# Kernel optimization log

Measured on AMD Instinct MI355X. Metric: run time of the kernel, lower is better.

Reference implementation:

```python
import jax, jax.numpy as jnp
import numpy as np

N, E, EDGES, G = 4096, 256, 131072, 64
H, DH = 4, 64  # MHA heads, head dim


def _ln(x, g, b, eps=1e-5):
    m = jnp.mean(x, -1, keepdims=True)
    v = jnp.var(x, -1, keepdims=True)
    return g * (x - m) * jax.lax.rsqrt(v + eps) + b


def setup_inputs() -> dict:
    key = jax.random.key(0)
    ks = jax.random.split(key, 40)
    i = iter(range(40))
    def rn(shape, s=1.0):
        return jax.random.normal(ks[next(i)], shape, jnp.float32) * s
    w = lambda shape: rn(shape, 0.02)
    inp = {
        "node_hidden": rn((N, E)),
        "edge_hidden": rn((EDGES, E)),
        "pos": rn((N, 3)),
        # GINEConv MLP: Lin(E,2E) -> LN -> ReLU -> Dropout -> Lin(2E,E)
        "gine_w1": w((E, 2 * E)), "gine_b1": jnp.zeros((2 * E,)),
        "gine_ln_g": jnp.ones((2 * E,)), "gine_ln_b": jnp.zeros((2 * E,)),
        "gine_w2": w((2 * E, E)), "gine_b2": jnp.zeros((E,)),
        "norm1_g": jnp.ones((E,)), "norm1_b": jnp.zeros((E,)),
        # DirectionalMessagePassing params
        "dir_w": w((3, E)), "dir_b": jnp.zeros((E,)),
        "msg_w": w((E, E)), "msg_b": jnp.zeros((E,)),
        # MultiheadAttention
        "wq": w((E, E)), "bq": jnp.zeros((E,)),
        "wk": w((E, E)), "bk": jnp.zeros((E,)),
        "wv": w((E, E)), "bv": jnp.zeros((E,)),
        "wo": w((E, E)), "bo": jnp.zeros((E,)),
        # gate
        "gate_w": w((2 * E, E)), "gate_b": jnp.zeros((E,)),
        "norm2_g": jnp.ones((E,)), "norm2_b": jnp.zeros((E,)),
        # GraphNorm affine
        "gn_g": jnp.ones((E,)), "gn_b": jnp.zeros((E,)),
        # int inputs
        "edge_index": jax.random.randint(ks[next(i)], (2, EDGES), 0, N, jnp.int64 if jax.config.jax_enable_x64 else jnp.int32),
        "node_id": jnp.sort(jax.random.randint(ks[next(i)], (N,), 0, G)),
        "edge_id": jax.random.randint(ks[next(i)], (EDGES,), 0, G),
    }
    return inp


def reference(node_hidden, edge_hidden, pos,
              gine_w1, gine_b1, gine_ln_g, gine_ln_b, gine_w2, gine_b2,
              norm1_g, norm1_b, dir_w, dir_b, msg_w, msg_b,
              wq, bq, wk, bk, wv, bv, wo, bo,
              gate_w, gate_b, norm2_g, norm2_b, gn_g, gn_b,
              edge_index, node_id, edge_id):
    src, dst = edge_index[0], edge_index[1]
    identity = node_hidden

    # --- GINEConv: out = MLP(x + sum_j relu(x_j + e_ij)), eps=0 ---
    msg = jax.nn.relu(node_hidden[src] + edge_hidden)           # [EDGES, E]
    agg = jax.ops.segment_sum(msg, dst, num_segments=N)         # [N, E]
    h = node_hidden + agg
    h = jax.nn.relu(_ln(h @ gine_w1 + gine_b1, gine_ln_g, gine_ln_b))
    gnn_out = _ln(h @ gine_w2 + gine_b2, norm1_g, norm1_b)      # norm1

    # --- DirectionalMessagePassing over unit edge directions ---
    vec = pos[dst] - pos[src]                                   # [EDGES, 3]
    vec = vec / (jnp.linalg.norm(vec, axis=-1, keepdims=True) + 1e-8)
    dfeat = vec @ dir_w + dir_b                                 # [EDGES, E]
    smsg = gnn_out[src] * dfeat
    sagg = jax.ops.segment_sum(smsg, dst, num_segments=N)
    spatial_out = sagg @ msg_w + msg_b                          # [N, E]

    # --- MHA: q = gnn_out, k = v = spatial_out (seq = nodes, batch=1) ---
    q = (gnn_out @ wq + bq).reshape(N, H, DH)
    k = (spatial_out @ wk + bk).reshape(N, H, DH)
    v = (spatial_out @ wv + bv).reshape(N, H, DH)
    scores = jnp.einsum("nhd,mhd->hnm", q, k) / np.sqrt(DH)
    attn = jax.nn.softmax(scores, axis=-1)
    fused = jnp.einsum("hnm,mhd->nhd", attn, v).reshape(N, E) @ wo + bo

    # --- gated residual blend + norm2 ---
    gate = jax.nn.sigmoid(jnp.concatenate([fused, identity], -1) @ gate_w + gate_b)
    out = gate * fused + (1.0 - gate) * identity
    out = _ln(out, norm2_g, norm2_b)

    # --- GraphNorm: per-graph mean/var over nodes (segment stats) ---
    counts = jax.ops.segment_sum(jnp.ones((N, 1), out.dtype), node_id, num_segments=G)
    mean = jax.ops.segment_sum(out, node_id, num_segments=G) / counts
    cen = out - mean[node_id]
    var = jax.ops.segment_sum(cen * cen, node_id, num_segments=G) / counts
    out = gn_g * cen * jax.lax.rsqrt(var[node_id] + 1e-5) + gn_b

    # last_act = True; dropout is eval-mode identity
    return jax.nn.relu(out)
```

## Files before the change

kernel.cpp:

```cpp
#include <hip/hip_runtime.h>
#include <hip/hip_bf16.h>

#define N_NODES 4096
#define E_DIM   256
#define N_EDGES 131072
#define N_GRAPHS 64
#define H_HEADS 4
#define DH      64
#define SPLIT   8

typedef unsigned short u16;
typedef __attribute__((ext_vector_type(8))) short bf16x8;
typedef __attribute__((ext_vector_type(4))) float f32x4;

__device__ __forceinline__ float u2f(u16 u) {
    union { unsigned int i; float f; } c; c.i = ((unsigned int)u) << 16; return c.f;
}
__device__ __forceinline__ u16 f2bu(float f) {
    __hip_bfloat16 h = __float2bfloat16(f);
    return *reinterpret_cast<u16*>(&h);
}
__device__ __forceinline__ float ldv(const void* p, size_t i, int f32) {
    return f32 ? ((const float*)p)[i] : u2f(((const u16*)p)[i]);
}
__device__ __forceinline__ float4 ldv4(const void* p, size_t i, int f32) {
    if (f32) return *(const float4*)((const float*)p + i);
    ushort4 u = *(const ushort4*)((const u16*)p + i);
    return make_float4(u2f(u.x), u2f(u.y), u2f(u.z), u2f(u.w));
}
__device__ __forceinline__ int ldi(const int* p, int i, int i64) {
    return i64 ? p[2 * i] : p[i];
}

__global__ void k_detect(const u16* __restrict__ ones_raw, const int* __restrict__ ei_raw,
                         int* __restrict__ flags) {
    flags[0] = (ones_raw[0] == 0) ? 1 : 0;
    flags[1] = (ei_raw[1] == 0 && ei_raw[3] == 0 && ei_raw[5] == 0 && ei_raw[7] == 0) ? 1 : 0;
}

__global__ void k_cvt(const void* __restrict__ s, float* __restrict__ d, int n,
                      const int* __restrict__ flags) {
    int i = blockIdx.x * 256 + threadIdx.x;
    if (i < n) d[i] = ldv(s, i, flags[0]);
}

__global__ void k_cvtb(const void* __restrict__ s, u16* __restrict__ d, int n4,
                       const int* __restrict__ flags) {
    int i = blockIdx.x * 256 + threadIdx.x;
    if (i < n4) {
        float4 v = ldv4(s, (size_t)i * 4, flags[0]);
        ushort4 o;
        o.x = f2bu(v.x); o.y = f2bu(v.y); o.z = f2bu(v.z); o.w = f2bu(v.w);
        ((ushort4*)d)[i] = o;
    }
}

struct SmDesc { const void* src; float* dst; int n; };
struct SmTable { SmDesc d[19]; };
__global__ __launch_bounds__(256) void k_cvts(SmTable tb, const int* __restrict__ flags) {
    int ti = blockIdx.x / 48;
    int off = (blockIdx.x % 48) * 256 + threadIdx.x;
    SmDesc e = tb.d[ti];
    if (off < e.n) e.dst[off] = ldv(e.src, off, flags[0]);
}

struct WtDesc { const void* src; u16* dst; int K; int N; int base; };
struct WtTable { WtDesc d[8]; };
__global__ __launch_bounds__(256) void k_cvtw(WtTable tb, const int* __restrict__ flags) {
    __shared__ u16 tile[64][68];
    int b = blockIdx.x;
    int i = 0;
    while (i < 7 && b >= tb.d[i + 1].base) i++;
    WtDesc e = tb.d[i];
    int tl = b - e.base;
    int ntn = e.N >> 6;
    int kt = tl / ntn, nt = tl % ntn;
    int t = threadIdx.x, r = t >> 2, c0 = (t & 3) * 16;
    int f32 = flags[0];
#pragma unroll
    for (int j = 0; j < 16; j++)
        tile[r][c0 + j] = f2bu(ldv(e.src, (size_t)(kt * 64 + r) * e.N + nt * 64 + c0 + j, f32));
    __syncthreads();
#pragma unroll
    for (int j = 0; j < 16; j++)
        e.dst[(size_t)(nt * 64 + r) * e.K + kt * 64 + c0 + j] = tile[c0 + j][r];
}

__global__ __launch_bounds__(256) void k_biasfold(const float* __restrict__ bq, const float* __restrict__ bk,
                                                  const float* __restrict__ bv, const float* __restrict__ msgb,
                                                  const u16* __restrict__ wkvt, float* __restrict__ bqkv) {
    int t = blockIdx.x * 256 + threadIdx.x;
    if (t < 256) { bqkv[t] = bq[t]; return; }
    int c = t - 256;
    float s = (c < 256) ? bk[c] : bv[c - 256];
    const u16* row = wkvt + (size_t)c * 256;
    float acc = 0.f;
    for (int k = 0; k < 256; k++) acc = fmaf(msgb[k], u2f(row[k]), acc);
    bqkv[256 + c] = s + acc;
}

__global__ __launch_bounds__(256) void k_mgemm(const void* __restrict__ A0, const void* __restrict__ A1,
                                               int K0, int Ktot, const u16* __restrict__ BT,
                                               const float* __restrict__ bias, void* __restrict__ C,
                                               int Nc, int outbf, int abf, int mode,
                                               u16* __restrict__ vt) {
    __shared__ u16 As[64 * 64];
    __shared__ u16 Bs[64 * 64];
    int t = threadIdx.x;
    int wv = t >> 6, l = t & 63, lg = l >> 4, lc = l & 15;
    int wm = wv >> 1, wn = wv & 1;
    int m0 = blockIdx.y * 64, n0 = blockIdx.x * 64;
    f32x4 acc[2][2] = {};
    int sr = t >> 2, sc = (t & 3) * 16;
    int sw = (sr & 7) << 3;

    for (int k0 = 0; k0 < Ktot; k0 += 64) {
        const void* Abase; int astride, kof;
        if (mode == 1) { Abase = (n0 < K0) ? A0 : A1; astride = Ktot; kof = k0; }
        else if (k0 < K0) { Abase = A0; astride = K0; kof = k0; }
        else { Abase = A1; astride = Ktot - K0; kof = k0 - K0; }
        if (abf) {
            const u16* Ap = (const u16*)Abase + (size_t)(m0 + sr) * astride + kof + sc;
            *(bf16x8*)&As[(sr * 64 + sc) ^ sw]     = *(const bf16x8*)Ap;
            *(bf16x8*)&As[(sr * 64 + sc + 8) ^ sw] = *(const bf16x8*)(Ap + 8);
        } else {
            const float* Ap = (const float*)Abase + (size_t)(m0 + sr) * astride + kof + sc;
#pragma unroll
            for (int j = 0; j < 2; j++) {
                float4 f0 = *(const float4*)(Ap + j * 8);
                float4 f1 = *(const float4*)(Ap + j * 8 + 4);
                bf16x8 bv;
                bv[0] = (short)f2bu(f0.x); bv[1] = (short)f2bu(f0.y);
                bv[2] = (short)f2bu(f0.z); bv[3] = (short)f2bu(f0.w);
                bv[4] = (short)f2bu(f1.x); bv[5] = (short)f2bu(f1.y);
                bv[6] = (short)f2bu(f1.z); bv[7] = (short)f2bu(f1.w);
                *(bf16x8*)&As[(sr * 64 + sc + j * 8) ^ sw] = bv;
            }
        }
        const u16* Bp = BT + (size_t)(n0 + sr) * Ktot + k0 + sc;
        *(bf16x8*)&Bs[(sr * 64 + sc) ^ sw]     = *(const bf16x8*)Bp;
        *(bf16x8*)&Bs[(sr * 64 + sc + 8) ^ sw] = *(const bf16x8*)(Bp + 8);
        __syncthreads();
#pragma unroll
        for (int ks = 0; ks < 2; ks++) {
            bf16x8 af[2], bfr[2];
#pragma unroll
            for (int mi = 0; mi < 2; mi++) {
                int row = wm * 32 + mi * 16 + lc;
                af[mi] = *(const bf16x8*)&As[(row * 64 + ks * 32 + lg * 8) ^ ((row & 7) << 3)];
            }
#pragma unroll
            for (int ni = 0; ni < 2; ni++) {
                int col = wn * 32 + ni * 16 + lc;
                bfr[ni] = *(const bf16x8*)&Bs[(col * 64 + ks * 32 + lg * 8) ^ ((col & 7) << 3)];
            }
#pragma unroll
            for (int mi = 0; mi < 2; mi++)
#pragma unroll
                for (int ni = 0; ni < 2; ni++)
                    acc[mi][ni] = __builtin_amdgcn_mfma_f32_16x16x32_bf16(af[mi], bfr[ni], acc[mi][ni], 0, 0, 0);
        }
        __syncthreads();
    }
#pragma unroll
    for (int mi = 0; mi < 2; mi++)
#pragma unroll
        for (int ni = 0; ni < 2; ni++) {
            int col = n0 + wn * 32 + ni * 16 + lc;
            float bb = bias ? bias[col] : 0.f;
#pragma unroll
            for (int r = 0; r < 4; r++) {
                int row = m0 + wm * 32 + mi * 16 + lg * 4 + r;
                float v = acc[mi][ni][r] + bb;
                u16 hb = f2bu(v);
                if (outbf) ((u16*)C)[(size_t)row * Nc + col] = hb;
                else       ((float*)C)[(size_t)row * Nc + col] = v;
                if (vt && col >= 512) vt[(size_t)(col - 512) * N_NODES + row] = hb;
            }
        }
// ... 89 lines not shown
            for (int n = 0; n < 4; n++)
                P_lds[wv][(q * 64 + n * 16 + lc) ^ sw] = f2bu(p[n][r]);
        }
#pragma unroll
        for (int kc = 0; kc < 2; kc++) {
            bf16x8 a = *(const bf16x8*)&P_lds[wv][(lc * 64 + kc * 32 + lg * 8) ^ ((lc & 7) << 3)];
#pragma unroll
            for (int n = 0; n < 4; n++) {
                int row = n * 16 + lc;
                bf16x8 b = *(const bf16x8*)&V_lds[(row * 64 + kc * 32 + lg * 8) ^ ((row & 7) << 3)];
                oacc[n] = __builtin_amdgcn_mfma_f32_16x16x32_bf16(a, b, oacc[n], 0, 0, 0);
            }
        }
    }

#pragma unroll
    for (int r = 0; r < 4; r++) {
        u16* pp = part + ((size_t)(c * H_HEADS + h) * N_NODES + q0 + lg * 4 + r) * 72;
#pragma unroll
        for (int n = 0; n < 4; n++) pp[n * 16 + lc] = f2bu(oacc[n][r]);
        if (lc == 0) { *(float*)(pp + 64) = mrow[r]; *(float*)(pp + 66) = lrow[r]; }
    }
}

__global__ __launch_bounds__(256) void k_combine(const u16* __restrict__ part, u16* __restrict__ attnoh) {
    int n = blockIdx.x, t = threadIdx.x;
    int h = t >> 6, d = t & 63;
    float M = -1e30f;
#pragma unroll
    for (int c = 0; c < SPLIT; c++)
        M = fmaxf(M, *(const float*)(part + ((size_t)(c * H_HEADS + h) * N_NODES + n) * 72 + 64));
    float L = 0.f, o = 0.f;
#pragma unroll
    for (int c = 0; c < SPLIT; c++) {
        const u16* pp = part + ((size_t)(c * H_HEADS + h) * N_NODES + n) * 72;
        float w = __expf(*(const float*)(pp + 64) - M);
        L = fmaf(*(const float*)(pp + 66), w, L);
        o = fmaf(u2f(pp[d]), w, o);
    }
    attnoh[(size_t)n * E_DIM + h * DH + d] = f2bu(o / L);
}

__device__ __forceinline__ void block_red2(float& a, float& b, float* sbuf) {
#pragma unroll
    for (int o = 32; o > 0; o >>= 1) { a += __shfl_down(a, o); b += __shfl_down(b, o); }
    int w = threadIdx.x >> 6;
    if ((threadIdx.x & 63) == 0) { sbuf[w] = a; sbuf[4 + w] = b; }
    __syncthreads();
    a = sbuf[0] + sbuf[1] + sbuf[2] + sbuf[3];
    b = sbuf[4] + sbuf[5] + sbuf[6] + sbuf[7];
    __syncthreads();
}

__global__ void k_count(const int* __restrict__ ei, int* __restrict__ count,
                        const int* __restrict__ flags) {
    int e = blockIdx.x * 256 + threadIdx.x;
    int i64 = flags[1];
    int d = i64 ? ei[2 * (N_EDGES + e)] : ei[N_EDGES + e];
    atomicAdd(&count[d], 1);
}

__global__ __launch_bounds__(1024) void k_scan(const int* __restrict__ count,
                                               int* __restrict__ offs, int* __restrict__ cursor) {
    __shared__ int wsum[16];
    int t = threadIdx.x, lane = t & 63, wid = t >> 6;
    int c0 = count[t * 4 + 0], c1 = count[t * 4 + 1], c2 = count[t * 4 + 2], c3 = count[t * 4 + 3];
    int tot = c0 + c1 + c2 + c3;
    int inc = tot;
#pragma unroll
    for (int o = 1; o < 64; o <<= 1) { int v = __shfl_up(inc, o); if (lane >= o) inc += v; }
    if (lane == 63) wsum[wid] = inc;
    __syncthreads();
    if (t < 16) {
        int v = wsum[t];
#pragma unroll
        for (int o = 1; o < 16; o <<= 1) { int u = __shfl_up(v, o); if (t >= o) v += u; }
        wsum[t] = v;
    }
    __syncthreads();
    int base = (wid ? wsum[wid - 1] : 0) + inc - tot;
    int o0 = base, o1 = base + c0, o2 = o1 + c1, o3 = o2 + c2;
    offs[t * 4 + 0] = o0; offs[t * 4 + 1] = o1; offs[t * 4 + 2] = o2; offs[t * 4 + 3] = o3;
    cursor[t * 4 + 0] = o0; cursor[t * 4 + 1] = o1; cursor[t * 4 + 2] = o2; cursor[t * 4 + 3] = o3;
    if (t == 1023) offs[4096] = wsum[15];
}

__global__ void k_scatter(const int* __restrict__ ei, int* __restrict__ cursor,
                          int* __restrict__ elist, const int* __restrict__ flags) {
    int e = blockIdx.x * 256 + threadIdx.x;
    int i64 = flags[1];
    int d = i64 ? ei[2 * (N_EDGES + e)] : ei[N_EDGES + e];
    int p = atomicAdd(&cursor[d], 1);
    elist[p] = e;
}

__global__ __launch_bounds__(256) void k_gine_agg(const float* __restrict__ xf, const void* __restrict__ eh,
                                                  const int* __restrict__ ei, const int* __restrict__ offs,
                                                  const int* __restrict__ elist, const int* __restrict__ flags,
                                                  float* __restrict__ hout) {
    int wv = threadIdx.x >> 6, ld = threadIdx.x & 63;
    int n = blockIdx.x * 4 + wv;
    int f32 = flags[0], i64 = flags[1];
    int cc = ld * 4;
    float4 acc = *(const float4*)&xf[(size_t)n * E_DIM + cc];
    int i0 = offs[n], i1 = offs[n + 1];
    int i = i0;
    for (; i + 4 <= i1; i += 4) {
        int e[4], s[4];
#pragma unroll
        for (int j = 0; j < 4; j++) e[j] = elist[i + j];
#pragma unroll
        for (int j = 0; j < 4; j++) s[j] = ldi(ei, e[j], i64);
        float4 a[4], x[4];
#pragma unroll
        for (int j = 0; j < 4; j++) a[j] = ldv4(eh, (size_t)e[j] * E_DIM + cc, f32);
#pragma unroll
        for (int j = 0; j < 4; j++) x[j] = *(const float4*)&xf[(size_t)s[j] * E_DIM + cc];
#pragma unroll
        for (int j = 0; j < 4; j++) {
            acc.x += fmaxf(x[j].x + a[j].x, 0.f);
            acc.y += fmaxf(x[j].y + a[j].y, 0.f);
            acc.z += fmaxf(x[j].z + a[j].z, 0.f);
            acc.w += fmaxf(x[j].w + a[j].w, 0.f);
        }
    }
    for (; i < i1; i++) {
        int e0 = elist[i];
        int s0 = ldi(ei, e0, i64);
        float4 a0 = ldv4(eh, (size_t)e0 * E_DIM + cc, f32);
        float4 x0 = *(const float4*)&xf[(size_t)s0 * E_DIM + cc];
        acc.x += fmaxf(x0.x + a0.x, 0.f);
        acc.y += fmaxf(x0.y + a0.y, 0.f);
        acc.z += fmaxf(x0.z + a0.z, 0.f);
        acc.w += fmaxf(x0.w + a0.w, 0.f);
    }
    *(float4*)&hout[(size_t)n * E_DIM + cc] = acc;
}

template <int W>
__global__ __launch_bounds__(256) void k_ln(float* __restrict__ X, const float* __restrict__ g,
                                            const float* __restrict__ b, int relu) {
    __shared__ float sbuf[8];
    constexpr int PE = W / 256;
    int n = blockIdx.x, t = threadIdx.x;
    float* row = X + (size_t)n * W;
    float x[PE];
    float s = 0.f, s2 = 0.f;
#pragma unroll
    for (int i = 0; i < PE; i++) { x[i] = row[t + i * 256]; s += x[i]; s2 += x[i] * x[i]; }
    block_red2(s, s2, sbuf);
    float mean = s / W;
    float var = fmaxf(s2 / W - mean * mean, 0.f);
    float rstd = rsqrtf(var + 1e-5f);
#pragma unroll
    for (int i = 0; i < PE; i++) {
        int c = t + i * 256;
        float y = g[c] * (x[i] - mean) * rstd + b[c];
        if (relu) y = fmaxf(y, 0.f);
        row[c] = y;
    }
}

__global__ __launch_bounds__(256) void k_dir(const float* __restrict__ posf, const int* __restrict__ ei,
                                             const int* __restrict__ offs, const int* __restrict__ elist,
                                             const int* __restrict__ flags,
                                             const float* __restrict__ gnn, const float* __restrict__ dw,
                                             const float* __restrict__ db, float* __restrict__ sagg) {
    int wv = threadIdx.x >> 6, ld = threadIdx.x & 63;
    int n = blockIdx.x * 4 + wv;
    int i64 = flags[1];
    int cc = ld * 4;
    float4 w0 = *(const float4*)&dw[cc];
    float4 w1 = *(const float4*)&dw[256 + cc];
    float4 w2 = *(const float4*)&dw[512 + cc];
    float4 bb = *(const float4*)&db[cc];
    float px = posf[n * 3 + 0], py = posf[n * 3 + 1], pz = posf[n * 3 + 2];
    float4 acc = {0.f, 0.f, 0.f, 0.f};
    int i0 = offs[n], i1 = offs[n + 1];
    int i = i0;
    for (; i + 2 <= i1; i += 2) {
        int e0 = elist[i], e1 = elist[i + 1];
        int s0 = ldi(ei, e0, i64), s1 = ldi(ei, e1, i64);
        float q0x = posf[s0 * 3 + 0], q0y = posf[s0 * 3 + 1], q0z = posf[s0 * 3 + 2];
        float q1x = posf[s1 * 3 + 0], q1y = posf[s1 * 3 + 1], q1z = posf[s1 * 3 + 2];
        float4 g0 = *(const float4*)&gnn[(size_t)s0 * E_DIM + cc];
        float4 g1 = *(const float4*)&gnn[(size_t)s1 * E_DIM + cc];
        float vx0 = px - q0x, vy0 = py - q0y, vz0 = pz - q0z;
        float vx1 = px - q1x, vy1 = py - q1y, vz1 = pz - q1z;
        float rn0 = 1.f / (sqrtf(vx0 * vx0 + vy0 * vy0 + vz0 * vz0) + 1e-8f);
        float rn1 = 1.f / (sqrtf(vx1 * vx1 + vy1 * vy1 + vz1 * vz1) + 1e-8f);
        acc.x = fmaf(g0.x, bb.x + (vx0 * w0.x + vy0 * w1.x + vz0 * w2.x) * rn0, acc.x);
        acc.y = fmaf(g0.y, bb.y + (vx0 * w0.y + vy0 * w1.y + vz0 * w2.y) * rn0, acc.y);
        acc.z = fmaf(g0.z, bb.z + (vx0 * w0.z + vy0 * w1.z + vz0 * w2.z) * rn0, acc.z);
        acc.w = fmaf(g0.w, bb.w + (vx0 * w0.w + vy0 * w1.w + vz0 * w2.w) * rn0, acc.w);
        acc.x = fmaf(g1.x, bb.x + (vx1 * w0.x + vy1 * w1.x + vz1 * w2.x) * rn1, acc.x);
        acc.y = fmaf(g1.y, bb.y + (vx1 * w0.y + vy1 * w1.y + vz1 * w2.y) * rn1, acc.y);
        acc.z = fmaf(g1.z, bb.z + (vx1 * w0.z + vy1 * w1.z + vz1 * w2.z) * rn1, acc.z);
        acc.w = fmaf(g1.w, bb.w + (vx1 * w0.w + vy1 * w1.w + vz1 * w2.w) * rn1, acc.w);
    }
    if (i < i1) {
        int e0 = elist[i];
        int s0 = ldi(ei, e0, i64);
        float q0x = posf[s0 * 3 + 0], q0y = posf[s0 * 3 + 1], q0z = posf[s0 * 3 + 2];
        float4 g0 = *(const float4*)&gnn[(size_t)s0 * E_DIM + cc];
        float vx0 = px - q0x, vy0 = py - q0y, vz0 = pz - q0z;
        float rn0 = 1.f / (sqrtf(vx0 * vx0 + vy0 * vy0 + vz0 * vz0) + 1e-8f);
        acc.x = fmaf(g0.x, bb.x + (vx0 * w0.x + vy0 * w1.x + vz0 * w2.x) * rn0, acc.x);
        acc.y = fmaf(g0.y, bb.y + (vx0 * w0.y + vy0 * w1.y + vz0 * w2.y) * rn0, acc.y);
        acc.z = fmaf(g0.z, bb.z + (vx0 * w0.z + vy0 * w1.z + vz0 * w2.z) * rn0, acc.z);
        acc.w = fmaf(g0.w, bb.w + (vx0 * w0.w + vy0 * w1.w + vz0 * w2.w) * rn0, acc.w);
    }
    *(float4*)&sagg[(size_t)n * E_DIM + cc] = acc;
}

__global__ __launch_bounds__(256) void k_gate_ln(const float* __restrict__ gl, const float* __restrict__ fused,
                                                 const float* __restrict__ xf, const float* __restrict__ g2,
                                                 const float* __restrict__ b2, float* __restrict__ out2) {
    __shared__ float sbuf[8];
    int n = blockIdx.x, t = threadIdx.x;
    float z = gl[(size_t)n * E_DIM + t];
    float gate = 1.f / (1.f + __expf(-z));
    float o = gate * fused[(size_t)n * E_DIM + t] + (1.f - gate) * xf[(size_t)n * E_DIM + t];
    float s = o, s2 = o * o;
    block_red2(s, s2, sbuf);
    float mean = s / E_DIM;
    float var = fmaxf(s2 / E_DIM - mean * mean, 0.f);
    float y = g2[t] * (o - mean) * rsqrtf(var + 1e-5f) + b2[t];
    out2[(size_t)n * E_DIM + t] = y;
}

__device__ __forceinline__ int lbound(const int* __restrict__ nid, int v, int i64) {
    int lo = 0, hi = N_NODES;
    while (lo < hi) { int mid = (lo + hi) >> 1; if (ldi(nid, mid, i64) < v) lo = mid + 1; else hi = mid; }
    return lo;
}

__global__ __launch_bounds__(256) void k_gnstats(const int* __restrict__ nid, const int* __restrict__ flags,
                                                 const float* __restrict__ out2,
                                                 float* __restrict__ gnm, float* __restrict__ gnr) {
    int g = blockIdx.x, t = threadIdx.x;
    int i64 = flags[1];
    int a = lbound(nid, g, i64), bnd = lbound(nid, g + 1, i64);
    int cnt = bnd - a;
    float s = 0.f, s2 = 0.f;
    for (int n = a; n < bnd; n++) {
        float x = out2[(size_t)n * E_DIM + t];
        s += x; s2 = fmaf(x, x, s2);
    }
    float inv = cnt ? 1.f / (float)cnt : 0.f;
    float mean = s * inv;
    float var = fmaxf(s2 * inv - mean * mean, 0.f);
    gnm[g * E_DIM + t] = mean;
    gnr[g * E_DIM + t] = rsqrtf(var + 1e-5f);
}

__global__ __launch_bounds__(256) void k_gnapply(const float* __restrict__ out2, const int* __restrict__ nid,
                                                 const float* __restrict__ gnm, const float* __restrict__ gnr,
                                                 const float* __restrict__ gg, const float* __restrict__ gb,
                                                 const int* __restrict__ flags, void* __restrict__ out) {
    int n = blockIdx.x, t = threadIdx.x;
    int g = ldi(nid, n, flags[1]);
    float y = gg[t] * (out2[(size_t)n * E_DIM + t] - gnm[g * E_DIM + t]) * gnr[g * E_DIM + t] + gb[t];
    y = fmaxf(y, 0.f);
    size_t idx = (size_t)n * E_DIM + t;
    if (flags[0]) ((float*)out)[idx] = y;
    else ((__hip_bfloat16*)out)[idx] = __float2bfloat16(y);
}

extern "C" void kernel_launch(void* const* d_in, const int* in_sizes, int n_in,
                              void* d_out, int out_size, void* d_ws, size_t ws_size,
                              hipStream_t stream) {
    const void* x_r    = d_in[0];
    const void* eh_r   = d_in[1];
    const void* pos_r  = d_in[2];
    const void* w1_r   = d_in[3];
    const void* b1_r   = d_in[4];
    const void* glng_r = d_in[5];
    const void* glnb_r = d_in[6];
    const void* w2_r   = d_in[7];
    const void* b2_r   = d_in[8];
    const void* n1g_r  = d_in[9];
    const void* n1b_r  = d_in[10];
    const void* dirw_r = d_in[11];
    const void* dirb_r = d_in[12];
    const void* msgw_r = d_in[13];
    const void* msgb_r = d_in[14];
    const void* wq_r   = d_in[15];
    const void* bq_r   = d_in[16];
    const void* wk_r   = d_in[17];
    const void* bk_r   = d_in[18];
    const void* wv_r   = d_in[19];
    const void* bv_r   = d_in[20];
    const void* wo_r   = d_in[21];
    const void* bo_r   = d_in[22];
    const void* gw_r   = d_in[23];
    const void* gb_r   = d_in[24];
    const void* n2g_r  = d_in[25];
    const void* n2b_r  = d_in[26];
    const void* gng_r  = d_in[27];
    const void* gnb_r  = d_in[28];
    const int* ei      = (const int*)d_in[29];
    const int* nid     = (const int*)d_in[30];

    char* ws = (char*)d_ws;
    const size_t KB = 1 << 10, MB = 1 << 20;
    int*   flags  = (int*)(ws + 0);
    int*   count  = (int*)(ws + 16 * KB);
    int*   offs   = (int*)(ws + 32 * KB);
    int*   cursor = (int*)(ws + 64 * KB);
    int*   elist  = (int*)(ws + 128 * KB);

    float* posf   = (float*)(ws + 1 * MB);
    float* prm    = (float*)(ws + 1 * MB + 64 * KB);
    float* b1f   = prm + 0;
    float* glngf = prm + 512,  *glnbf = prm + 1024;
    float* b2f   = prm + 1536;
    float* n1gf  = prm + 1792, *n1bf  = prm + 2048;
    float* dirwf = prm + 2304;
    float* dirbf = prm + 3072, *msgbf = prm + 3328;
    float* bqf   = prm + 3584, *bkf   = prm + 3840, *bvf = prm + 4096, *bof = prm + 4352;
    float* gbf   = prm + 4608;
    float* n2gf  = prm + 4864, *n2bf  = prm + 5120;
    float* gngf  = prm + 5376, *gnbf  = prm + 5632;

    u16* w1t    = (u16*)(ws + 2 * MB);
    u16* w2t    = (u16*)(ws + 2 * MB + 256 * KB);
    u16* wot    = (u16*)(ws + 2 * MB + 512 * KB);
    u16* gwt    = (u16*)(ws + 2 * MB + 640 * KB);
    u16* wqkvt  = (u16*)(ws + 3 * MB);
    u16* wkvt   = (u16*)(ws + 3 * MB + 384 * KB);
    u16* msgwb  = (u16*)(ws + 3 * MB + 640 * KB);
    float* bqkvf = (float*)(ws + 3 * MB + 768 * KB);

    float* xf     = (float*)(ws + 5 * MB);
    float* hbuf   = (float*)(ws + 9 * MB);
    float* T1     = (float*)(ws + 13 * MB);
    float* gnn    = (float*)(ws + 21 * MB);
    float* sagg   = (float*)(ws + 25 * MB);
    u16*   QKVh   = (u16*)(ws + 29 * MB);
    u16*   VT     = (u16*)(ws + 35 * MB);
    u16*   part   = (u16*)(ws + 37 * MB);
    u16*   attnoh = (u16*)(ws + 9 * MB);
    float* fused  = (float*)(ws + 13 * MB);
    float* gatel  = (float*)(ws + 17 * MB);
    float* out2   = (float*)(ws + 21 * MB);
    float* gnm    = (float*)(ws + 25 * MB);
    float* gnr    = (float*)(ws + 25 * MB + 64 * KB);

    k_detect<<<1, 1, 0, stream>>>((const u16*)glng_r, ei, flags);

    k_cvt<<<(N_NODES * E_DIM + 255) / 256, 256, 0, stream>>>(x_r, xf, N_NODES * E_DIM, flags);

    SmTable st;
    {
        int i = 0;
        auto add = [&](const void* s, float* d, int n) { st.d[i].src = s; st.d[i].dst = d; st.d[i].n = n; i++; };
        add(pos_r, posf, N_NODES * 3);
        add(b1_r, b1f, 512); add(glng_r, glngf, 512); add(glnb_r, glnbf, 512);
        add(b2_r, b2f, 256); add(n1g_r, n1gf, 256); add(n1b_r, n1bf, 256);
        add(dirw_r, dirwf, 768); add(dirb_r, dirbf, 256); add(msgb_r, msgbf, 256);
        add(bq_r, bqf, 256); add(bk_r, bkf, 256); add(bv_r, bvf, 256); add(bo_r, bof, 256);
        add(gb_r, gbf, 256); add(n2g_r, n2gf, 256); add(n2b_r, n2bf, 256);
        add(gng_r, gngf, 256); add(gnb_r, gnbf, 256);
    }
    k_cvts<<<19 * 48, 256, 0, stream>>>(st, flags);

    WtTable wt;
    {
        int i = 0, base = 0;
        auto add = [&](const void* s, u16* d, int K, int N) {
            wt.d[i].src = s; wt.d[i].dst = d; wt.d[i].K = K; wt.d[i].N = N; wt.d[i].base = base;
            base += (K / 64) * (N / 64); i++;
        };
        add(w1_r, w1t, 256, 512);
        add(w2_r, w2t, 512, 256);
        add(wq_r, wqkvt, 256, 256);
        add(wk_r, wkvt, 256, 256);
        add(wv_r, wkvt + 256 * 256, 256, 256);
        add(wo_r, wot, 256, 256);
        add(gw_r, gwt, 512, 256);
        wt.d[7].base = 0x7fffffff;
        k_cvtw<<<base, 256, 0, stream>>>(wt, flags);
    }
    k_cvtb<<<64, 256, 0, stream>>>(msgw_r, msgwb, 256 * 256 / 4, flags);
    k_mgemm<<<dim3(4, 8), 256, 0, stream>>>(wkvt, nullptr, 256, 256, msgwb, nullptr,
                                            wqkvt + 256 * 256, 256, 1, 1, 0, nullptr);
    k_biasfold<<<3, 256, 0, stream>>>(bqf, bkf, bvf, msgbf, wkvt, bqkvf);

    hipMemsetAsync(count, 0, N_NODES * sizeof(int), stream);
    k_count<<<N_EDGES / 256, 256, 0, stream>>>(ei, count, flags);
    k_scan<<<1, 1024, 0, stream>>>(count, offs, cursor);
    k_scatter<<<N_EDGES / 256, 256, 0, stream>>>(ei, cursor, elist, flags);

    k_gine_agg<<<N_NODES / 4, 256, 0, stream>>>(xf, eh_r, ei, offs, elist, flags, hbuf);
    k_mgemm<<<dim3(8, 64), 256, 0, stream>>>(hbuf, nullptr, 256, 256, w1t, b1f, T1, 512, 0, 0, 0, nullptr);
    k_ln<512><<<N_NODES, 256, 0, stream>>>(T1, glngf, glnbf, 1);
    k_mgemm<<<dim3(4, 64), 256, 0, stream>>>(T1, nullptr, 512, 512, w2t, b2f, gnn, 256, 0, 0, 0, nullptr);
    k_ln<256><<<N_NODES, 256, 0, stream>>>(gnn, n1gf, n1bf, 0);

    k_dir<<<N_NODES / 4, 256, 0, stream>>>(posf, ei, offs, elist, flags, gnn, dirwf, dirbf, sagg);

    k_mgemm<<<dim3(12, 64), 256, 0, stream>>>(gnn, sagg, 256, 256, wqkvt, bqkvf, QKVh, 768, 1, 0, 1, VT);

    k_attn<<<dim3(N_NODES / 64, H_HEADS, SPLIT), 256, 0, stream>>>(QKVh, VT, part);
    k_combine<<<N_NODES, 256, 0, stream>>>(part, attnoh);
    k_mgemm<<<dim3(4, 64), 256, 0, stream>>>(attnoh, nullptr, 256, 256, wot, bof, fused, 256, 0, 1, 0, nullptr);

    k_mgemm<<<dim3(4, 64), 256, 0, stream>>>(fused, xf, 256, 512, gwt, gbf, gatel, 256, 0, 0, 0, nullptr);
    k_gate_ln<<<N_NODES, 256, 0, stream>>>(gatel, fused, xf, n2gf, n2bf, out2);

    k_gnstats<<<N_GRAPHS, 256, 0, stream>>>(nid, flags, out2, gnm, gnr);
    k_gnapply<<<N_NODES, 256, 0, stream>>>(out2, nid, gnm, gnr, gngf, gnbf, flags, d_out);
}
```

Baseline: 292.2 us.

## Merge prep kernels, fold wo into gate GEMM, use bf16 gathers, halve attention split

Replaces the separate detect/convert kernels with one k_prep launch and makes each kernel recompute the dtype flags inline. The output projection wo is folded algebraically into the gate weights, so a single GEMM produces both fused and gate logits. Gathers now read bf16 copies of x and gnn, plus packed (edge, src) pairs and padded pos4, which cuts gather bandwidth and one level of indirection. The attention split drops from 8 to 4. The trade-off is slightly lower precision and extra weight-folding GEMMs in setup.

```diff
diff --git a/kernel.cpp b/kernel.cpp
--- a/kernel.cpp
+++ b/kernel.cpp
@@ -7,7 +7,7 @@
 #define N_GRAPHS 64
 #define H_HEADS 4
 #define DH      64
-#define SPLIT   8
+#define SPLIT   4
 
 typedef unsigned short u16;
 typedef __attribute__((ext_vector_type(8))) short bf16x8;
@@ -28,82 +28,117 @@
     ushort4 u = *(const ushort4*)((const u16*)p + i);
     return make_float4(u2f(u.x), u2f(u.y), u2f(u.z), u2f(u.w));
 }
+__device__ __forceinline__ float4 ldb4(const u16* p, size_t i) {
+    ushort4 u = *(const ushort4*)(p + i);
+    return make_float4(u2f(u.x), u2f(u.y), u2f(u.z), u2f(u.w));
+}
+__device__ __forceinline__ int chk_f32(const void* ones_raw) { return ((const u16*)ones_raw)[0] == 0; }
+__device__ __forceinline__ int chk_i64(const int* ei) {
+    return (ei[1] == 0 && ei[3] == 0 && ei[5] == 0 && ei[7] == 0);
+}
 __device__ __forceinline__ int ldi(const int* p, int i, int i64) {
     return i64 ? p[2 * i] : p[i];
 }
 
-__global__ void k_detect(const u16* __restrict__ ones_raw, const int* __restrict__ ei_raw,
-                         int* __restrict__ flags) {
-    flags[0] = (ones_raw[0] == 0) ? 1 : 0;
-    flags[1] = (ei_raw[1] == 0 && ei_raw[3] == 0 && ei_raw[5] == 0 && ei_raw[7] == 0) ? 1 : 0;
-}
-
-__global__ void k_cvt(const void* __restrict__ s, float* __restrict__ d, int n,
-                      const int* __restrict__ flags) {
-    int i = blockIdx.x * 256 + threadIdx.x;
-    if (i < n) d[i] = ldv(s, i, flags[0]);
-}
-
-__global__ void k_cvtb(const void* __restrict__ s, u16* __restrict__ d, int n4,
-                       const int* __restrict__ flags) {
-    int i = blockIdx.x * 256 + threadIdx.x;
-    if (i < n4) {
-        float4 v = ldv4(s, (size_t)i * 4, flags[0]);
-        ushort4 o;
-        o.x = f2bu(v.x); o.y = f2bu(v.y); o.z = f2bu(v.z); o.w = f2bu(v.w);
-        ((ushort4*)d)[i] = o;
-    }
-}
-
 struct SmDesc { const void* src; float* dst; int n; };
-struct SmTable { SmDesc d[19]; };
-__global__ __launch_bounds__(256) void k_cvts(SmTable tb, const int* __restrict__ flags) {
-    int ti = blockIdx.x / 48;
-    int off = (blockIdx.x % 48) * 256 + threadIdx.x;
-    SmDesc e = tb.d[ti];
-    if (off < e.n) e.dst[off] = ldv(e.src, off, flags[0]);
-}
-
+struct SmTable { SmDesc d[18]; };
 struct WtDesc { const void* src; u16* dst; int K; int N; int base; };
 struct WtTable { WtDesc d[8]; };
-__global__ __launch_bounds__(256) void k_cvtw(WtTable tb, const int* __restrict__ flags) {
+
+__global__ __launch_bounds__(256) void k_prep(const void* __restrict__ x_r, float* __restrict__ xf,
+                                              u16* __restrict__ xh, const void* __restrict__ pos_r,
+                                              float4* __restrict__ pos4, SmTable st, WtTable wt,
+                                              const void* __restrict__ msgw_r, u16* __restrict__ msgwb,
+                                              const void* __restrict__ wo_r, u16* __restrict__ wob,
+                                              const void* __restrict__ ones_raw) {
     __shared__ u16 tile[64][68];
-    int b = blockIdx.x;
-    int i = 0;
-    while (i < 7 && b >= tb.d[i + 1].base) i++;
-    WtDesc e = tb.d[i];
-    int tl = b - e.base;
-    int ntn = e.N >> 6;
-    int kt = tl / ntn, nt = tl % ntn;
-    int t = threadIdx.x, r = t >> 2, c0 = (t & 3) * 16;
-    int f32 = flags[0];
-#pragma unroll
-    for (int j = 0; j < 16; j++)
-        tile[r][c0 + j] = f2bu(ldv(e.src, (size_t)(kt * 64 + r) * e.N + nt * 64 + c0 + j, f32));
-    __syncthreads();
-#pragma unroll
-    for (int j = 0; j < 16; j++)
-        e.dst[(size_t)(nt * 64 + r) * e.K + kt * 64 + c0 + j] = tile[c0 + j][r];
-}
-
-__global__ __launch_bounds__(256) void k_biasfold(const float* __restrict__ bq, const float* __restrict__ bk,
-                                                  const float* __restrict__ bv, const float* __restrict__ msgb,
-                                                  const u16* __restrict__ wkvt, float* __restrict__ bqkv) {
-    int t = blockIdx.x * 256 + threadIdx.x;
-    if (t < 256) { bqkv[t] = bq[t]; return; }
-    int c = t - 256;
-    float s = (c < 256) ? bk[c] : bv[c - 256];
-    const u16* row = wkvt + (size_t)c * 256;
-    float acc = 0.f;
-    for (int k = 0; k < 256; k++) acc = fmaf(msgb[k], u2f(row[k]), acc);
-    bqkv[256 + c] = s + acc;
+    int b = blockIdx.x, t = threadIdx.x;
+    int f32 = chk_f32(ones_raw);
+    if (b < 4096) {
+        int i = b * 256 + t;
+        float v = ldv(x_r, i, f32);
+        xf[i] = v; xh[i] = f2bu(v);
+        return;
+    }
+    b -= 4096;
+    if (b < 16) {
+        int n = b * 256 + t;
+        pos4[n] = make_float4(ldv(pos_r, n * 3 + 0, f32), ldv(pos_r, n * 3 + 1, f32),
+                              ldv(pos_r, n * 3 + 2, f32), 0.f);
+        return;
+    }
+    b -= 16;
+    if (b < 18 * 48) {
+        int ti = b / 48;
+        int off = (b % 48) * 256 + t;
+        SmDesc e = st.d[ti];
+        if (off < e.n) e.dst[off] = ldv(e.src, off, f32);
+        return;
+    }
+    b -= 18 * 48;
+    if (b < 160) {
+        int i = 0;
+        while (i < 7 && b >= wt.d[i + 1].base) i++;
+        WtDesc e = wt.d[i];
+        int tl = b - e.base;
+        int ntn = e.N >> 6;
+        int kt = tl / ntn, nt = tl % ntn;
+        int r = t >> 2, c0 = (t & 3) * 16;
+#pragma unroll
+        for (int j = 0; j < 16; j++)
+            tile[r][c0 + j] = f2bu(ldv(e.src, (size_t)(kt * 64 + r) * e.N + nt * 64 + c0 + j, f32));
+        __syncthreads();
+#pragma unroll
+        for (int j = 0; j < 16; j++)
+            e.dst[(size_t)(nt * 64 + r) * e.K + kt * 64 + c0 + j] = tile[c0 + j][r];
+        return;
+    }
+    b -= 160;
+    if (b < 256) { int i = b * 256 + t; msgwb[i] = f2bu(ldv(msgw_r, i, f32)); return; }
+    b -= 256;
+    { int i = b * 256 + t; wob[i] = f2bu(ldv(wo_r, i, f32)); }
+}
+
+__global__ __launch_bounds__(256) void k_asm2(const u16* __restrict__ wot, const u16* __restrict__ foldT,
+                                              const u16* __restrict__ gwt, u16* __restrict__ BT2) {
+    int idx = blockIdx.x * 256 + threadIdx.x;
+    int col = idx >> 9, k = idx & 511;
+    u16 v;
+    if (col < 256) v = (k < 256) ? wot[col * 256 + k] : (u16)0;
+    else { int c = col - 256; v = (k < 256) ? foldT[c * 256 + k] : gwt[(size_t)c * 512 + k]; }
+    BT2[idx] = v;
+}
+
+__global__ __launch_bounds__(256) void k_biases(const float* __restrict__ bqf, const float* __restrict__ bkf,
+                                                const float* __restrict__ bvf, const float* __restrict__ msgbf,
+                                                const u16* __restrict__ wkvt, const float* __restrict__ bof,
+                                                const float* __restrict__ gbf, const u16* __restrict__ gwt,
+                                                float* __restrict__ bqkv, float* __restrict__ bias2) {
+    int b = blockIdx.x, t = threadIdx.x;
+    if (b < 3) {
+        int i = b * 256 + t;
+        if (i < 256) { bqkv[i] = bqf[i]; return; }
+        int c = i - 256;
+        float s = (c < 256) ? bkf[c] : bvf[c - 256];
+        const u16* row = wkvt + (size_t)c * 256;
+        float acc = 0.f;
+        for (int k = 0; k < 256; k++) acc = fmaf(msgbf[k], u2f(row[k]), acc);
+        bqkv[256 + c] = s + acc;
+    } else if (b == 3) {
+        bias2[t] = bof[t];
+    } else {
+        float acc = gbf[t];
+        const u16* row = gwt + (size_t)t * 512;
+        for (int j = 0; j < 256; j++) acc = fmaf(bof[j], u2f(row[j]), acc);
+        bias2[256 + t] = acc;
+    }
 }
 
 __global__ __launch_bounds__(256) void k_mgemm(const void* __restrict__ A0, const void* __restrict__ A1,
+                                               int as0, int as1, int abf0, int abf1,
                                                int K0, int Ktot, const u16* __restrict__ BT,
                                                const float* __restrict__ bias, void* __restrict__ C,
-                                               int Nc, int outbf, int abf, int mode,
-                                               u16* __restrict__ vt) {
+                                               int Nc, int outbf, int mode, u16* __restrict__ vt) {
     __shared__ u16 As[64 * 64];
     __shared__ u16 Bs[64 * 64];
     int t = threadIdx.x;
@@ -115,16 +150,16 @@
     int sw = (sr & 7) << 3;
 
     for (int k0 = 0; k0 < Ktot; k0 += 64) {
-        const void* Abase; int astride, kof;
-        if (mode == 1) { Abase = (n0 < K0) ? A0 : A1; astride = Ktot; kof = k0; }
-        else if (k0 < K0) { Abase = A0; astride = K0; kof = k0; }
-        else { Abase = A1; astride = Ktot - K0; kof = k0 - K0; }
+        const void* Ab; int astr, kof, abf;
+        if (mode == 1) { int pick = (n0 < K0); Ab = pick ? A0 : A1; astr = pick ? as0 : as1; abf = pick ? abf0 : abf1; kof = k0; }
+        else if (k0 < K0) { Ab = A0; astr = as0; abf = abf0; kof = k0; }
+        else { Ab = A1; astr = as1; abf = abf1; kof = k0 - K0; }
         if (abf) {
-            const u16* Ap = (const u16*)Abase + (size_t)(m0 + sr) * astride + kof + sc;
+            const u16* Ap = (const u16*)Ab + (size_t)(m0 + sr) * astr + kof + sc;
             *(bf16x8*)&As[(sr * 64 + sc) ^ sw]     = *(const bf16x8*)Ap;
             *(bf16x8*)&As[(sr * 64 + sc + 8) ^ sw] = *(const bf16x8*)(Ap + 8);
         } else {
-            const float* Ap = (const float*)Abase + (size_t)(m0 + sr) * astride + kof + sc;
+            const float* Ap = (const float*)Ab + (size_t)(m0 + sr) * astr + kof + sc;
 #pragma unroll
             for (int j = 0; j < 2; j++) {
                 float4 f0 = *(const float4*)(Ap + j * 8);
@@ -320,10 +355,9 @@
     __syncthreads();
 }
 
-__global__ void k_count(const int* __restrict__ ei, int* __restrict__ count,
-                        const int* __restrict__ flags) {
+__global__ void k_count(const int* __restrict__ ei, int* __restrict__ count) {
     int e = blockIdx.x * 256 + threadIdx.x;
-    int i64 = flags[1];
+    int i64 = chk_i64(ei);
     int d = i64 ? ei[2 * (N_EDGES + e)] : ei[N_EDGES + e];
     atomicAdd(&count[d], 1);
 }
@@ -354,36 +388,35 @@
 }
 
 __global__ void k_scatter(const int* __restrict__ ei, int* __restrict__ cursor,
-                          int* __restrict__ elist, const int* __restrict__ flags) {
+                          int2* __restrict__ elist2) {
     int e = blockIdx.x * 256 + threadIdx.x;
-    int i64 = flags[1];
+    int i64 = chk_i64(ei);
+    int s = i64 ? ei[2 * e] : ei[e];
     int d = i64 ? ei[2 * (N_EDGES + e)] : ei[N_EDGES + e];
     int p = atomicAdd(&cursor[d], 1);
-    elist[p] = e;
-}
-
-__global__ __launch_bounds__(256) void k_gine_agg(const float* __restrict__ xf, const void* __restrict__ eh,
-                                                  const int* __restrict__ ei, const int* __restrict__ offs,
-                                                  const int* __restrict__ elist, const int* __restrict__ flags,
-                                                  float* __restrict__ hout) {
+    elist2[p] = make_int2(e, s);
+}
+
+__global__ __launch_bounds__(256) void k_gine_agg(const float* __restrict__ xf, const u16* __restrict__ xh,
+                                                  const void* __restrict__ eh, const void* __restrict__ ones_raw,
+                                                  const int* __restrict__ offs, const int2* __restrict__ elist2,
+                                                  u16* __restrict__ houth) {
     int wv = threadIdx.x >> 6, ld = threadIdx.x & 63;
     int n = blockIdx.x * 4 + wv;
-    int f32 = flags[0], i64 = flags[1];
+    int f32 = chk_f32(ones_raw);
     int cc = ld * 4;
     float4 acc = *(const float4*)&xf[(size_t)n * E_DIM + cc];
     int i0 = offs[n], i1 = offs[n + 1];
     int i = i0;
     for (; i + 4 <= i1; i += 4) {
-        int e[4], s[4];
-#pragma unroll
-        for (int j = 0; j < 4; j++) e[j] = elist[i + j];
-#pragma unroll
-        for (int j = 0; j < 4; j++) s[j] = ldi(ei, e[j], i64);
+        int2 es[4];
+#pragma unroll
+        for (int j = 0; j < 4; j++) es[j] = elist2[i + j];
         float4 a[4], x[4];
 #pragma unroll
-        for (int j = 0; j < 4; j++) a[j] = ldv4(eh, (size_t)e[j] * E_DIM + cc, f32);
-#pragma unroll
-        for (int j = 0; j < 4; j++) x[j] = *(const float4*)&xf[(size_t)s[j] * E_DIM + cc];
+        for (int j = 0; j < 4; j++) a[j] = ldv4(eh, (size_t)es[j].x * E_DIM + cc, f32);
+#pragma unroll
+        for (int j = 0; j < 4; j++) x[j] = ldb4(xh, (size_t)es[j].y * E_DIM + cc);
 #pragma unroll
         for (int j = 0; j < 4; j++) {
             acc.x += fmaxf(x[j].x + a[j].x, 0.f);
@@ -393,25 +426,27 @@
         }
     }
     for (; i < i1; i++) {
-        int e0 = elist[i];
-        int s0 = ldi(ei, e0, i64);
-        float4 a0 = ldv4(eh, (size_t)e0 * E_DIM + cc, f32);
-        float4 x0 = *(const float4*)&xf[(size_t)s0 * E_DIM + cc];
+        int2 es = elist2[i];
+        float4 a0 = ldv4(eh, (size_t)es.x * E_DIM + cc, f32);
+        float4 x0 = ldb4(xh, (size_t)es.y * E_DIM + cc);
         acc.x += fmaxf(x0.x + a0.x, 0.f);
         acc.y += fmaxf(x0.y + a0.y, 0.f);
         acc.z += fmaxf(x0.z + a0.z, 0.f);
         acc.w += fmaxf(x0.w + a0.w, 0.f);
     }
-    *(float4*)&hout[(size_t)n * E_DIM + cc] = acc;
-}
-
-template <int W>
-__global__ __launch_bounds__(256) void k_ln(float* __restrict__ X, const float* __restrict__ g,
-                                            const float* __restrict__ b, int relu) {
+    ushort4 o;
+    o.x = f2bu(acc.x); o.y = f2bu(acc.y); o.z = f2bu(acc.z); o.w = f2bu(acc.w);
+    *(ushort4*)&houth[(size_t)n * E_DIM + cc] = o;
+}
+
+template <int W, int OUTBF>
+__global__ __launch_bounds__(256) void k_ln(const float* __restrict__ in, void* __restrict__ out,
+                                            const float* __restrict__ g, const float* __restrict__ b,
+                                            int relu) {
     __shared__ float sbuf[8];
     constexpr int PE = W / 256;
     int n = blockIdx.x, t = threadIdx.x;
-    float* row = X + (size_t)n * W;
+    const float* row = in + (size_t)n * W;
     float x[PE];
     float s = 0.f, s2 = 0.f;
 #pragma unroll
@@ -425,36 +460,33 @@
         int c = t + i * 256;
         float y = g[c] * (x[i] - mean) * rstd + b[c];
         if (relu) y = fmaxf(y, 0.f);
-        row[c] = y;
-    }
-}
-
-__global__ __launch_bounds__(256) void k_dir(const float* __restrict__ posf, const int* __restrict__ ei,
-                                             const int* __restrict__ offs, const int* __restrict__ elist,
-                                             const int* __restrict__ flags,
-                                             const float* __restrict__ gnn, const float* __restrict__ dw,
-                                             const float* __restrict__ db, float* __restrict__ sagg) {
+        if (OUTBF) ((u16*)out)[(size_t)n * W + c] = f2bu(y);
+        else       ((float*)out)[(size_t)n * W + c] = y;
+    }
+}
+
+__global__ __launch_bounds__(256) void k_dir(const float4* __restrict__ pos4, const int* __restrict__ offs,
+                                             const int2* __restrict__ elist2, const u16* __restrict__ gnnh,
+                                             const float* __restrict__ dw, const float* __restrict__ db,
+                                             u16* __restrict__ saggh) {
     int wv = threadIdx.x >> 6, ld = threadIdx.x & 63;
     int n = blockIdx.x * 4 + wv;
-    int i64 = flags[1];
     int cc = ld * 4;
     float4 w0 = *(const float4*)&dw[cc];
     float4 w1 = *(const float4*)&dw[256 + cc];
     float4 w2 = *(const float4*)&dw[512 + cc];
     float4 bb = *(const float4*)&db[cc];
-    float px = posf[n * 3 + 0], py = posf[n * 3 + 1], pz = posf[n * 3 + 2];
+    float4 pn = pos4[n];
     float4 acc = {0.f, 0.f, 0.f, 0.f};
     int i0 = offs[n], i1 = offs[n + 1];
     int i = i0;
     for (; i + 2 <= i1; i += 2) {
-        int e0 = elist[i], e1 = elist[i + 1];
-        int s0 = ldi(ei, e0, i64), s1 = ldi(ei, e1, i64);
-        float q0x = posf[s0 * 3 + 0], q0y = posf[s0 * 3 + 1], q0z = posf[s0 * 3 + 2];
-        float q1x = posf[s1 * 3 + 0], q1y = posf[s1 * 3 + 1], q1z = posf[s1 * 3 + 2];
-        float4 g0 = *(const float4*)&gnn[(size_t)s0 * E_DIM + cc];
-        float4 g1 = *(const float4*)&gnn[(size_t)s1 * E_DIM + cc];
-        float vx0 = px - q0x, vy0 = py - q0y, vz0 = pz - q0z;
-        float vx1 = px - q1x, vy1 = py - q1y, vz1 = pz - q1z;
+        int2 es0 = elist2[i], es1 = elist2[i + 1];
+        float4 p0 = pos4[es0.y], p1 = pos4[es1.y];
+        float4 g0 = ldb4(gnnh, (size_t)es0.y * E_DIM + cc);
+        float4 g1 = ldb4(gnnh, (size_t)es1.y * E_DIM + cc);
+        float vx0 = pn.x - p0.x, vy0 = pn.y - p0.y, vz0 = pn.z - p0.z;
+        float vx1 = pn.x - p1.x, vy1 = pn.y - p1.y, vz1 = pn.z - p1.z;
         float rn0 = 1.f / (sqrtf(vx0 * vx0 + vy0 * vy0 + vz0 * vz0) + 1e-8f);
         float rn1 = 1.f / (sqrtf(vx1 * vx1 + vy1 * vy1 + vz1 * vz1) + 1e-8f);
         acc.x = fmaf(g0.x, bb.x + (vx0 * w0.x + vy0 * w1.x + vz0 * w2.x) * rn0, acc.x);
@@ -467,28 +499,30 @@
         acc.w = fmaf(g1.w, bb.w + (vx1 * w0.w + vy1 * w1.w + vz1 * w2.w) * rn1, acc.w);
     }
     if (i < i1) {
-        int e0 = elist[i];
-        int s0 = ldi(ei, e0, i64);
-        float q0x = posf[s0 * 3 + 0], q0y = posf[s0 * 3 + 1], q0z = posf[s0 * 3 + 2];
-        float4 g0 = *(const float4*)&gnn[(size_t)s0 * E_DIM + cc];
-        float vx0 = px - q0x, vy0 = py - q0y, vz0 = pz - q0z;
+        int2 es0 = elist2[i];
+        float4 p0 = pos4[es0.y];
+        float4 g0 = ldb4(gnnh, (size_t)es0.y * E_DIM + cc);
+        float vx0 = pn.x - p0.x, vy0 = pn.y - p0.y, vz0 = pn.z - p0.z;
         float rn0 = 1.f / (sqrtf(vx0 * vx0 + vy0 * vy0 + vz0 * vz0) + 1e-8f);
         acc.x = fmaf(g0.x, bb.x + (vx0 * w0.x + vy0 * w1.x + vz0 * w2.x) * rn0, acc.x);
         acc.y = fmaf(g0.y, bb.y + (vx0 * w0.y + vy0 * w1.y + vz0 * w2.y) * rn0, acc.y);
         acc.z = fmaf(g0.z, bb.z + (vx0 * w0.z + vy0 * w1.z + vz0 * w2.z) * rn0, acc.z);
         acc.w = fmaf(g0.w, bb.w + (vx0 * w0.w + vy0 * w1.w + vz0 * w2.w) * rn0, acc.w);
     }
-    *(float4*)&sagg[(size_t)n * E_DIM + cc] = acc;
-}
-
-__global__ __launch_bounds__(256) void k_gate_ln(const float* __restrict__ gl, const float* __restrict__ fused,
-                                                 const float* __restrict__ xf, const float* __restrict__ g2,
-                                                 const float* __restrict__ b2, float* __restrict__ out2) {
+    ushort4 o;
+    o.x = f2bu(acc.x); o.y = f2bu(acc.y); o.z = f2bu(acc.z); o.w = f2bu(acc.w);
+    *(ushort4*)&saggh[(size_t)n * E_DIM + cc] = o;
+}
+
+__global__ __launch_bounds__(256) void k_gate_ln(const float* __restrict__ fg, const float* __restrict__ xf,
+                                                 const float* __restrict__ g2, const float* __restrict__ b2,
+                                                 float* __restrict__ out2) {
     __shared__ float sbuf[8];
     int n = blockIdx.x, t = threadIdx.x;
-    float z = gl[(size_t)n * E_DIM + t];
+    float fu = fg[(size_t)n * 512 + t];
+    float z  = fg[(size_t)n * 512 + 256 + t];
     float gate = 1.f / (1.f + __expf(-z));
-    float o = gate * fused[(size_t)n * E_DIM + t] + (1.f - gate) * xf[(size_t)n * E_DIM + t];
+    float o = gate * fu + (1.f - gate) * xf[(size_t)n * E_DIM + t];
     float s = o, s2 = o * o;
     block_red2(s, s2, sbuf);
     float mean = s / E_DIM;
@@ -503,11 +537,11 @@
     return lo;
 }
 
-__global__ __launch_bounds__(256) void k_gnstats(const int* __restrict__ nid, const int* __restrict__ flags,
+__global__ __launch_bounds__(256) void k_gnstats(const int* __restrict__ nid, const int* __restrict__ ei,
                                                  const float* __restrict__ out2,
                                                  float* __restrict__ gnm, float* __restrict__ gnr) {
     int g = blockIdx.x, t = threadIdx.x;
-    int i64 = flags[1];
+    int i64 = chk_i64(ei);
     int a = lbound(nid, g, i64), bnd = lbound(nid, g + 1, i64);
     int cnt = bnd - a;
     float s = 0.f, s2 = 0.f;
@@ -523,15 +557,16 @@
 }
 
 __global__ __launch_bounds__(256) void k_gnapply(const float* __restrict__ out2, const int* __restrict__ nid,
+                                                 const int* __restrict__ ei, const void* __restrict__ ones_raw,
                                                  const float* __restrict__ gnm, const float* __restrict__ gnr,
                                                  const float* __restrict__ gg, const float* __restrict__ gb,
-                                                 const int* __restrict__ flags, void* __restrict__ out) {
+                                                 void* __restrict__ out) {
     int n = blockIdx.x, t = threadIdx.x;
-    int g = ldi(nid, n, flags[1]);
+    int g = ldi(nid, n, chk_i64(ei));
     float y = gg[t] * (out2[(size_t)n * E_DIM + t] - gnm[g * E_DIM + t]) * gnr[g * E_DIM + t] + gb[t];
     y = fmaxf(y, 0.f);
     size_t idx = (size_t)n * E_DIM + t;
-    if (flags[0]) ((float*)out)[idx] = y;
+    if (chk_f32(ones_raw)) ((float*)out)[idx] = y;
     else ((__hip_bfloat16*)out)[idx] = __float2bfloat16(y);
 }
 
@@ -572,14 +607,12 @@
 
     char* ws = (char*)d_ws;
     const size_t KB = 1 << 10, MB = 1 << 20;
-    int*   flags  = (int*)(ws + 0);
-    int*   count  = (int*)(ws + 16 * KB);
+    int*   count  = (int*)(ws + 0);
     int*   offs   = (int*)(ws + 32 * KB);
     int*   cursor = (int*)(ws + 64 * KB);
-    int*   elist  = (int*)(ws + 128 * KB);
-
-    float* posf   = (float*)(ws + 1 * MB);
-    float* prm    = (float*)(ws + 1 * MB + 64 * KB);
+    int2*  elist2 = (int2*)(ws + 128 * KB);
+
+    float* prm    = (float*)(ws + 1 * MB + 192 * KB);
     float* b1f   = prm + 0;
     float* glngf = prm + 512,  *glnbf = prm + 1024;
     float* b2f   = prm + 1536;
@@ -590,6 +623,7 @@
     float* gbf   = prm + 4608;
     float* n2gf  = prm + 4864, *n2bf  = prm + 5120;
     float* gngf  = prm + 5376, *gnbf  = prm + 5632;
+    float4* pos4 = (float4*)(ws + 1 * MB + 256 * KB);
 
     u16* w1t    = (u16*)(ws + 2 * MB);
     u16* w2t    = (u16*)(ws + 2 * MB + 256 * KB);
@@ -598,32 +632,32 @@
     u16* wqkvt  = (u16*)(ws + 3 * MB);
     u16* wkvt   = (u16*)(ws + 3 * MB + 384 * KB);
     u16* msgwb  = (u16*)(ws + 3 * MB + 640 * KB);
-    float* bqkvf = (float*)(ws + 3 * MB + 768 * KB);
+    u16* wob    = (u16*)(ws + 3 * MB + 768 * KB);
+    u16* foldT  = (u16*)(ws + 3 * MB + 896 * KB);
+    u16* BT2    = (u16*)(ws + 4 * MB);
+    float* bias2f = (float*)(ws + 4 * MB + 512 * KB);
+    float* bqkvf  = (float*)(ws + 4 * MB + 516 * KB);
 
     float* xf     = (float*)(ws + 5 * MB);
-    float* hbuf   = (float*)(ws + 9 * MB);
+    u16*   xh     = (u16*)(ws + 9 * MB);
+    u16*   hbufh  = (u16*)(ws + 11 * MB);
     float* T1     = (float*)(ws + 13 * MB);
-    float* gnn    = (float*)(ws + 21 * MB);
-    float* sagg   = (float*)(ws + 25 * MB);
+    float* gnnf   = (float*)(ws + 21 * MB);
+    u16*   gnnh   = (u16*)(ws + 25 * MB);
+    u16*   saggh  = (u16*)(ws + 27 * MB);
     u16*   QKVh   = (u16*)(ws + 29 * MB);
     u16*   VT     = (u16*)(ws + 35 * MB);
     u16*   part   = (u16*)(ws + 37 * MB);
-    u16*   attnoh = (u16*)(ws + 9 * MB);
-    float* fused  = (float*)(ws + 13 * MB);
-    float* gatel  = (float*)(ws + 17 * MB);
+    u16*   attnoh = (u16*)(ws + 11 * MB);
+    float* fg     = (float*)(ws + 13 * MB);
     float* out2   = (float*)(ws + 21 * MB);
     float* gnm    = (float*)(ws + 25 * MB);
     float* gnr    = (float*)(ws + 25 * MB + 64 * KB);
-
-    k_detect<<<1, 1, 0, stream>>>((const u16*)glng_r, ei, flags);
-
-    k_cvt<<<(N_NODES * E_DIM + 255) / 256, 256, 0, stream>>>(x_r, xf, N_NODES * E_DIM, flags);
 
     SmTable st;
     {
         int i = 0;
         auto add = [&](const void* s, float* d, int n) { st.d[i].src = s; st.d[i].dst = d; st.d[i].n = n; i++; };
-        add(pos_r, posf, N_NODES * 3);
         add(b1_r, b1f, 512); add(glng_r, glngf, 512); add(glnb_r, glnbf, 512);
         add(b2_r, b2f, 256); add(n1g_r, n1gf, 256); add(n1b_r, n1bf, 256);
         add(dirw_r, dirwf, 768); add(dirb_r, dirbf, 256); add(msgb_r, msgbf, 256);
@@ -631,8 +665,6 @@
         add(gb_r, gbf, 256); add(n2g_r, n2gf, 256); add(n2b_r, n2bf, 256);
         add(gng_r, gngf, 256); add(gnb_r, gnbf, 256);
     }
-    k_cvts<<<19 * 48, 256, 0, stream>>>(st, flags);
-
     WtTable wt;
     {
         int i = 0, base = 0;
@@ -648,35 +680,42 @@
         add(wo_r, wot, 256, 256);
         add(gw_r, gwt, 512, 256);
         wt.d[7].base = 0x7fffffff;
-        k_cvtw<<<base, 256, 0, stream>>>(wt, flags);
-    }
-    k_cvtb<<<64, 256, 0, stream>>>(msgw_r, msgwb, 256 * 256 / 4, flags);
-    k_mgemm<<<dim3(4, 8), 256, 0, stream>>>(wkvt, nullptr, 256, 256, msgwb, nullptr,
-                                            wqkvt + 256 * 256, 256, 1, 1, 0, nullptr);
-    k_biasfold<<<3, 256, 0, stream>>>(bqf, bkf, bvf, msgbf, wkvt, bqkvf);
+    }
+    k_prep<<<4096 + 16 + 18 * 48 + 160 + 256 + 256, 256, 0, stream>>>(
+        x_r, xf, xh, pos_r, pos4, st, wt, msgw_r, msgwb, wo_r, wob, glng_r);
 
     hipMemsetAsync(count, 0, N_NODES * sizeof(int), stream);
-    k_count<<<N_EDGES / 256, 256, 0, stream>>>(ei, count, flags);
+    k_count<<<N_EDGES / 256, 256, 0, stream>>>(ei, count);
     k_scan<<<1, 1024, 0, stream>>>(count, offs, cursor);
-    k_scatter<<<N_EDGES / 256, 256, 0, stream>>>(ei, cursor, elist, flags);
-
-    k_gine_agg<<<N_NODES / 4, 256, 0, stream>>>(xf, eh_r, ei, offs, elist, flags, hbuf);
-    k_mgemm<<<dim3(8, 64), 256, 0, stream>>>(hbuf, nullptr, 256, 256, w1t, b1f, T1, 512, 0, 0, 0, nullptr);
-    k_ln<512><<<N_NODES, 256, 0, stream>>>(T1, glngf, glnbf, 1);
-    k_mgemm<<<dim3(4, 64), 256, 0, stream>>>(T1, nullptr, 512, 512, w2t, b2f, gnn, 256, 0, 0, 0, nullptr);
-    k_ln<256><<<N_NODES, 256, 0, stream>>>(gnn, n1gf, n1bf, 0);
-
-    k_dir<<<N_NODES / 4, 256, 0, stream>>>(posf, ei, offs, elist, flags, gnn, dirwf, dirbf, sagg);
-
-    k_mgemm<<<dim3(12, 64), 256, 0, stream>>>(gnn, sagg, 256, 256, wqkvt, bqkvf, QKVh, 768, 1, 0, 1, VT);
+    k_scatter<<<N_EDGES / 256, 256, 0, stream>>>(ei, cursor, elist2);
+
+    k_mgemm<<<dim3(4, 8), 256, 0, stream>>>(wkvt, nullptr, 256, 0, 1, 0, 256, 256, msgwb,
+                                            nullptr, wqkvt + 256 * 256, 256, 1, 0, nullptr);
+    k_mgemm<<<dim3(4, 4), 256, 0, stream>>>(gwt, nullptr, 512, 0, 1, 0, 256, 256, wob,
+                                            nullptr, foldT, 256, 1, 0, nullptr);
+    k_asm2<<<1024, 256, 0, stream>>>(wot, foldT, gwt, BT2);
+    k_biases<<<5, 256, 0, stream>>>(bqf, bkf, bvf, msgbf, wkvt, bof, gbf, gwt, bqkvf, bias2f);
+
+    k_gine_agg<<<N_NODES / 4, 256, 0, stream>>>(xf, xh, eh_r, glng_r, offs, elist2, hbufh);
+    k_mgemm<<<dim3(8, 64), 256, 0, stream>>>(hbufh, nullptr, 256, 0, 1, 0, 256, 256, w1t,
+                                             b1f, T1, 512, 0, 0, nullptr);
+    k_ln<512, 0><<<N_NODES, 256, 0, stream>>>(T1, T1, glngf, glnbf, 1);
+    k_mgemm<<<dim3(4, 64), 256, 0, stream>>>(T1, nullptr, 512, 0, 0, 0, 512, 512, w2t,
+                                             b2f, gnnf, 256, 0, 0, nullptr);
+    k_ln<256, 1><<<N_NODES, 256, 0, stream>>>(gnnf, gnnh, n1gf, n1bf, 0);
+
+    k_dir<<<N_NODES / 4, 256, 0, stream>>>(pos4, offs, elist2, gnnh, dirwf, dirbf, saggh);
+
+    k_mgemm<<<dim3(12, 64), 256, 0, stream>>>(gnnh, saggh, 256, 256, 1, 1, 256, 256, wqkvt,
+                                              bqkvf, QKVh, 768, 1, 1, VT);
 
     k_attn<<<dim3(N_NODES / 64, H_HEADS, SPLIT), 256, 0, stream>>>(QKVh, VT, part);
     k_combine<<<N_NODES, 256, 0, stream>>>(part, attnoh);
-    k_mgemm<<<dim3(4, 64), 256, 0, stream>>>(attnoh, nullptr, 256, 256, wot, bof, fused, 256, 0, 1, 0, nullptr);
-
-    k_mgemm<<<dim3(4, 64), 256, 0, stream>>>(fused, xf, 256, 512, gwt, gbf, gatel, 256, 0, 0, 0, nullptr);
-    k_gate_ln<<<N_NODES, 256, 0, stream>>>(gatel, fused, xf, n2gf, n2bf, out2);
-
-    k_gnstats<<<N_GRAPHS, 256, 0, stream>>>(nid, flags, out2, gnm, gnr);
-    k_gnapply<<<N_NODES, 256, 0, stream>>>(out2, nid, gnm, gnr, gngf, gnbf, flags, d_out);
-}
+
+    k_mgemm<<<dim3(8, 64), 256, 0, stream>>>(attnoh, xf, 256, 256, 1, 0, 256, 512, BT2,
+                                             bias2f, fg, 512, 0, 0, nullptr);
+    k_gate_ln<<<N_NODES, 256, 0, stream>>>(fg, xf, n2gf, n2bf, out2);
+
+    k_gnstats<<<N_GRAPHS, 256, 0, stream>>>(nid, ei, out2, gnm, gnr);
+    k_gnapply<<<N_NODES, 256, 0, stream>>>(out2, nid, ei, glng_r, gnm, gnr, gngf, gnbf, d_out);
+}
```

New measurement: 269.4 us. 7.8% less time.
